# Performance work log

Measured on AMD Instinct MI355X. Metric: run time of the kernel, lower is better.

## Reference

```python
import jax, jax.numpy as jnp
import numpy as np

D_MODEL = 1024
NHEAD = 16
HEAD_DIM = D_MODEL // NHEAD


def setup_inputs() -> dict:
    key = jax.random.key(0)
    ks = jax.random.split(key, 6)
    scale = 0.02
    x = jax.random.normal(ks[0], (8, 1024, D_MODEL), dtype=jnp.float32)
    # nn.Linear weights are [out, in]; per-head q/k/v stacked over heads
    W_split = jax.random.normal(ks[1], (D_MODEL, D_MODEL), dtype=jnp.float32) * scale
    W_out = jax.random.normal(ks[2], (D_MODEL, D_MODEL), dtype=jnp.float32) * scale
    Wq = jax.random.normal(ks[3], (NHEAD, HEAD_DIM, HEAD_DIM), dtype=jnp.float32) * scale
    Wk = jax.random.normal(ks[4], (NHEAD, HEAD_DIM, HEAD_DIM), dtype=jnp.float32) * scale
    Wv = jax.random.normal(ks[5], (NHEAD, HEAD_DIM, HEAD_DIM), dtype=jnp.float32) * scale
    return {"x": x, "W_split": W_split, "W_out": W_out, "Wq": Wq, "Wk": Wk, "Wv": Wv}


def reference(x, W_split, W_out, Wq, Wk, Wv):
    b, s, _ = x.shape
    # x_proj: [b, s, h, hd]
    xp = (x @ W_split.T).reshape(b, s, NHEAD, HEAD_DIM)
    # per-head Linear (weight [out,in]): y = x @ W.T
    q = jnp.einsum('bshd,hod->bsho', xp, Wq)
    k = jnp.einsum('bshd,hod->bsho', xp, Wk)
    v = jnp.einsum('bshd,hod->bsho', xp, Wv)
    # scores scaled by sqrt(head_dim) (Attention.d_model == head_dim)
    scores = jnp.einsum('bsho,btho->bhst', q, k) / jnp.sqrt(jnp.float32(HEAD_DIM))
    attn = jax.nn.softmax(scores, axis=-1)  # [b, h, s, s]
    out = jnp.einsum('bhst,btho->bsho', attn, v)  # [b, s, h, hd]
    concat = out.reshape(b, s, D_MODEL)
    return concat @ W_out.T
```

## Files before the change

### kernel.cpp

```cpp
#include <hip/hip_runtime.h>
#include <math.h>

#define NHEAD 16
#define HD 64
#define DMODEL 1024
#define SEQ 1024
#define BATCH 8
#define ROWS (BATCH * SEQ)

typedef __attribute__((ext_vector_type(8))) short bf16x8;
typedef __attribute__((ext_vector_type(8))) short short8v;
typedef __attribute__((ext_vector_type(4))) float f32x4;
typedef __attribute__((ext_vector_type(16))) float f32x16;
typedef __attribute__((ext_vector_type(4))) short short4v;
typedef __attribute__((ext_vector_type(4))) unsigned int uint32x4;

__device__ __forceinline__ unsigned short f2bf(float f) {
    unsigned u = __builtin_bit_cast(unsigned, f);
    u += 0x7FFF + ((u >> 16) & 1);
    return (unsigned short)(u >> 16);
}

__device__ __forceinline__ float fexp2(float x) {
#if __has_builtin(__builtin_amdgcn_exp2f)
    return __builtin_amdgcn_exp2f(x);
#else
    return __expf(x * 0.6931471805599453f);
#endif
}

__device__ __forceinline__ void gload16(const void* g, void* l) {
    __builtin_amdgcn_global_load_lds(
        (const __attribute__((address_space(1))) unsigned int*)g,
        (__attribute__((address_space(3))) unsigned int*)l, 16, 0, 0);
}

__global__ __launch_bounds__(256) void cvt_bf16(const float* __restrict__ src,
                                                unsigned short* __restrict__ dst,
                                                int n, float scale) {
    int i = (blockIdx.x * 256 + threadIdx.x) * 8;
    if (i >= n) return;
    float4 a = *(const float4*)(src + i);
    float4 b = *(const float4*)(src + i + 4);
    short8v o;
    o[0] = (short)f2bf(a.x * scale); o[1] = (short)f2bf(a.y * scale);
    o[2] = (short)f2bf(a.z * scale); o[3] = (short)f2bf(a.w * scale);
    o[4] = (short)f2bf(b.x * scale); o[5] = (short)f2bf(b.y * scale);
    o[6] = (short)f2bf(b.z * scale); o[7] = (short)f2bf(b.w * scale);
    *(short8v*)(dst + i) = o;
}

__global__ __launch_bounds__(256) void gemm1_qkv(const unsigned short* __restrict__ A,
                                                 const unsigned short* __restrict__ B,
                                                 const unsigned short* __restrict__ wqb,
                                                 const unsigned short* __restrict__ wkb,
                                                 const unsigned short* __restrict__ wvb,
                                                 unsigned short* __restrict__ qb,
                                                 unsigned short* __restrict__ kbuf,
                                                 unsigned short* __restrict__ vT) {
    __shared__ char lds[65536];
    const int tid  = threadIdx.x;
    const int w    = tid >> 6;
    const int lane = tid & 63;
    const int lr   = lane & 15, lg = lane >> 4;
    const int wr   = w >> 1,  wc = w & 1;
    const int m0   = blockIdx.y * 128;
    const int n0   = blockIdx.x * 128;
    const int K    = DMODEL;

    f32x4 acc[4][4] = {};

    const int srow   = lane >> 3;
    const int swbyte = ((lane & 7) ^ srow) << 4;

#define G1_STAGE(buf, k0)                                                          \
    {                                                                              \
        _Pragma("unroll")                                                          \
        for (int c = 0; c < 4; ++c) {                                              \
            int chunk = w * 4 + c;                                                 \
            int row   = chunk * 8 + srow;                                          \
            gload16((const char*)A + ((size_t)(m0 + row) * K + (k0)) * 2 + swbyte, \
                    lds + (buf) * 16384 + chunk * 1024);                           \
            gload16((const char*)B + ((size_t)(n0 + row) * K + (k0)) * 2 + swbyte, \
                    lds + 32768 + (buf) * 16384 + chunk * 1024);                   \
        }                                                                          \
    }

    G1_STAGE(0, 0);
    __syncthreads();

    int cur = 0;
    for (int t = 0; t < K / 64; ++t) {
        if (t + 1 < K / 64) G1_STAGE(cur ^ 1, (t + 1) * 64);

#pragma unroll
        for (int k2 = 0; k2 < 2; ++k2) {
            bf16x8 af[4], bg[4];
#pragma unroll
            for (int f = 0; f < 4; ++f) {
                int row = wr * 64 + f * 16 + lr;
                af[f] = *(const bf16x8*)(lds + cur * 16384 + row * 128 +
                                         ((k2 * 64 + lg * 16) ^ ((row & 7) << 4)));
            }
#pragma unroll
            for (int g = 0; g < 4; ++g) {
                int row = wc * 64 + g * 16 + lr;
                bg[g] = *(const bf16x8*)(lds + 32768 + cur * 16384 + row * 128 +
                                         ((k2 * 64 + lg * 16) ^ ((row & 7) << 4)));
            }
#pragma unroll
            for (int f = 0; f < 4; ++f)
#pragma unroll
                for (int g = 0; g < 4; ++g)
                    acc[f][g] = __builtin_amdgcn_mfma_f32_16x16x32_bf16(af[f], bg[g],
                                                                        acc[f][g], 0, 0, 0);
        }
        __syncthreads();
        cur ^= 1;
    }
#undef G1_STAGE

#pragma unroll
    for (int f = 0; f < 4; ++f)
#pragma unroll
        for (int g = 0; g < 4; ++g)
#pragma unroll
            for (int r = 0; r < 4; ++r) {
                int mrow = wr * 64 + f * 16 + lg * 4 + r;
                int ncol = wc * 64 + g * 16 + lr;
                *(unsigned short*)(lds + mrow * 256 + ((ncol * 2) ^ ((mrow & 7) << 4))) =
                    f2bf(acc[f][g][r]);
            }

    const int b  = m0 >> 10;
    const int sl = m0 & 1023;

#pragma unroll
    for (int hh = 0; hh < 2; ++hh) {
        const int h = blockIdx.x * 2 + hh;
#pragma unroll
        for (int i = 0; i < 6; ++i) {
            int c   = w * 6 + i;
            int p   = c >> 3, rc = c & 7;
            int row = rc * 8 + srow;
            const unsigned short* ws = (p == 0) ? wqb : (p == 1) ? wkb : wvb;
            gload16((const char*)ws + ((size_t)(h * 64 + row) * 64) * 2 + swbyte,
                    lds + 32768 + p * 8192 + rc * 1024);
        }
        __syncthreads();

        f32x4 a2[3][2][4] = {};
#pragma unroll
        for (int k2 = 0; k2 < 2; ++k2) {
            bf16x8 af[2];
#pragma unroll
            for (int f = 0; f < 2; ++f) {
                int row = w * 32 + f * 16 + lr;
                af[f] = *(const bf16x8*)(lds + row * 256 +
                                         ((hh * 128 + k2 * 64 + lg * 16) ^ ((row & 7) << 4)));
            }
#pragma unroll
            for (int p = 0; p < 3; ++p)
#pragma unroll
                for (int g = 0; g < 4; ++g) {
                    int o = g * 16 + lr;
                    bf16x8 bg = *(const bf16x8*)(lds + 32768 + p * 8192 + o * 128 +
                                                 ((k2 * 64 + lg * 16) ^ ((o & 7) << 4)));
#pragma unroll
                    for (int f = 0; f < 2; ++f)
                        a2[p][f][g] = __builtin_amdgcn_mfma_f32_16x16x32_bf16(af[f], bg,
                                                                              a2[p][f][g], 0, 0, 0);
                }
        }

#pragma unroll
        for (int f = 0; f < 2; ++f)
#pragma unroll
            for (int g = 0; g < 4; ++g) {
#pragma unroll
                for (int r = 0; r < 4; ++r) {
                    size_t idx = (size_t)(m0 + w * 32 + f * 16 + lg * 4 + r) * DMODEL +
                                 h * 64 + g * 16 + lr;
                    qb[idx]   = f2bf(a2[0][f][g][r]);
                    kbuf[idx] = f2bf(a2[1][f][g][r]);
                }
                short4v pv;
#pragma unroll
                for (int r = 0; r < 4; ++r) pv[r] = (short)f2bf(a2[2][f][g][r]);
                size_t o = (size_t)(b * 16 + h) * 64 + g * 16 + lr;
                *(short4v*)(vT + o * SEQ + sl + w * 32 + f * 16 + lg * 4) = pv;
            }
        __syncthreads();
    }
}

__global__ __launch_bounds__(256) void gemm_bf16(const unsigned short* __restrict__ A,
                                                 const unsigned short* __restrict__ B,
                                                 float* __restrict__ Cf,
                                                 int M, int N, int K) {
    __shared__ char sA[2][16384];
    __shared__ char sB[2][16384];
    const int tid  = threadIdx.x;
    const int w    = tid >> 6;
    const int lane = tid & 63;
    const int lr   = lane & 15, lg = lane >> 4;
    const int wr   = w >> 1,  wc = w & 1;
    const int m0   = blockIdx.y * 128;
    const int n0   = blockIdx.x * 128;

    f32x4 acc[4][4] = {};

    const int srow   = lane >> 3;
    const int swbyte = ((lane & 7) ^ srow) << 4;
    const int nt     = K / 64;

#define GEMM_STAGE(buf, k0)                                                        \
    {                                                                              \
        _Pragma("unroll")                                                          \
        for (int c = 0; c < 4; ++c) {                                              \
            int chunk = w * 4 + c;                                                 \
            int row   = chunk * 8 + srow;                                          \
            gload16((const char*)A + ((size_t)(m0 + row) * K + (k0)) * 2 + swbyte, \
                    sA[buf] + chunk * 1024);                                       \
            gload16((const char*)B + ((size_t)(n0 + row) * K + (k0)) * 2 + swbyte, \
                    sB[buf] + chunk * 1024);                                       \
        }                                                                          \
    }

    GEMM_STAGE(0, 0);
    __syncthreads();

    int cur = 0;
    for (int t = 0; t < nt; ++t) {
        if (t + 1 < nt) GEMM_STAGE(cur ^ 1, (t + 1) * 64);

#pragma unroll
        for (int k2 = 0; k2 < 2; ++k2) {
            bf16x8 af[4], bg[4];
#pragma unroll
            for (int f = 0; f < 4; ++f) {
                int row = wr * 64 + f * 16 + lr;
                af[f] = *(const bf16x8*)(sA[cur] + row * 128 +
                                         ((k2 * 64 + lg * 16) ^ ((row & 7) << 4)));
            }
#pragma unroll
            for (int g = 0; g < 4; ++g) {
                int row = wc * 64 + g * 16 + lr;
                bg[g] = *(const bf16x8*)(sB[cur] + row * 128 +
                                         ((k2 * 64 + lg * 16) ^ ((row & 7) << 4)));
            }
#pragma unroll
            for (int f = 0; f < 4; ++f)
#pragma unroll
                for (int g = 0; g < 4; ++g)
                    acc[f][g] = __builtin_amdgcn_mfma_f32_16x16x32_bf16(af[f], bg[g],
                                                                        acc[f][g], 0, 0, 0);
        }
        __syncthreads();
        cur ^= 1;
    }
#undef GEMM_STAGE

#pragma unroll
    for (int f = 0; f < 4; ++f)
#pragma unroll
        for (int g = 0; g < 4; ++g)
#pragma unroll
            for (int r = 0; r < 4; ++r)
                Cf[(size_t)(m0 + wr * 64 + f * 16 + lg * 4 + r) * N +
                   n0 + wc * 64 + g * 16 + lr] = acc[f][g][r];
}

__global__ __launch_bounds__(512) void attn_mfma(const unsigned short* __restrict__ qb,
                                                 const unsigned short* __restrict__ kb,
                                                 const unsigned short* __restrict__ vT,
                                                 unsigned short* __restrict__ ob) {
    __shared__ unsigned short sK[2][4096];
    __shared__ unsigned short sV[2][4096];

    const int tid  = threadIdx.x;
    const int w    = tid >> 6;
    const int lane = tid & 63;
    const int ql   = lane & 31;
    const int hl   = lane >> 5;
    const int bh   = blockIdx.y;
    const int b    = bh >> 4, h = bh & 15;
    const int s0   = blockIdx.x * 256;

    const unsigned short* qrow = qb + ((size_t)(b * SEQ + s0 + w * 32 + ql) * DMODEL + h * 64);
    bf16x8 qf[4];
#pragma unroll
    for (int s = 0; s < 4; ++s)
        qf[s] = *(const bf16x8*)(qrow + 16 * s + 8 * hl);

    f32x16 acc0 = {}, acc1 = {};
    float m_ = -1e30f, l_ = 0.f;

    const int srow = lane >> 3;
    const int ssw  = ((lane & 7) << 4) ^ (srow << 4);
    const int swz  = (ql & 7) << 4;

#define ATTN_STAGE(buf, kt)                                                          \
    {                                                                                \
        int row = w * 8 + srow;                                                      \
        gload16((const char*)kb +                                                    \
                    (((size_t)(b * SEQ + (kt) * 64 + row) * DMODEL + h * 64) * 2) + ssw, \
                (char*)sK[buf] + w * 1024);                                          \
        gload16((const char*)vT +                                                    \
                    (((size_t)(bh * 64 + row) * SEQ + (kt) * 64) * 2) + ssw,         \
                (char*)sV[buf] + w * 1024);                                          \
    }

    ATTN_STAGE(0, 0);
    __syncthreads();

    int cur = 0;
    for (int kt = 0; kt < SEQ / 64; ++kt) {
        if (kt + 1 < SEQ / 64) ATTN_STAGE(cur ^ 1, kt + 1);

        f32x16 st0 = {}, st1 = {};
        __builtin_amdgcn_s_setprio(1);
#pragma unroll
        for (int s = 0; s < 4; ++s) {
            int byo = (32 * s + 16 * hl) ^ swz;
            bf16x8 kf0 = *(const bf16x8*)((const char*)sK[cur] + ql * 128 + byo);
            bf16x8 kf1 = *(const bf16x8*)((const char*)sK[cur] + (32 + ql) * 128 + byo);
            st0 = __builtin_amdgcn_mfma_f32_32x32x16_bf16(kf0, qf[s], st0, 0, 0, 0);
            st1 = __builtin_amdgcn_mfma_f32_32x32x16_bf16(kf1, qf[s], st1, 0, 0, 0);
        }
        __builtin_amdgcn_s_setprio(0);

        float mx = st0[0];
#pragma unroll
        for (int i = 1; i < 16; ++i) mx = fmaxf(mx, st0[i]);
#pragma unroll
        for (int i = 0; i < 16; ++i) mx = fmaxf(mx, st1[i]);
        if (__any(mx > m_ + 8.f)) {
            float rm = fmaxf(mx, __shfl_xor(mx, 32, 64));
            float mn = fmaxf(m_, rm);
            float al = fexp2(m_ - mn);
            m_ = mn;
            l_ *= al;
#pragma unroll
            for (int i = 0; i < 16; ++i) { acc0[i] *= al; acc1[i] *= al; }
        }

        bf16x8 pf[4];
        float lsum = 0.f;
#define TILE_P(stv, PF0, PF1)                                                       \
        {                                                                           \
            float p_[16];                                                           \
            _Pragma("unroll")                                                       \
            for (int i = 0; i < 16; ++i) {                                          \
                p_[i] = fexp2(stv[i] - m_);                                         \
                lsum += p_[i];                                                      \
            }                                                                       \
            unsigned pk_[8];                                                        \
            _Pragma("unroll")                                                       \
            for (int i = 0; i < 8; ++i)                                             \
                asm("v_cvt_pk_bf16_f32 %0, %1, %2"                                  \
                    : "=v"(pk_[i]) : "v"(p_[2 * i]), "v"(p_[2 * i + 1]));           \
            auto rA = __builtin_amdgcn_permlane32_swap(pk_[0], pk_[2], false, false); \
            auto rB = __builtin_amdgcn_permlane32_swap(pk_[1], pk_[3], false, false); \
            auto rC = __builtin_amdgcn_permlane32_swap(pk_[4], pk_[6], false, false); \
            auto rD = __builtin_amdgcn_permlane32_swap(pk_[5], pk_[7], false, false); \
            uint32x4 f0, f1;                                                        \
            f0[0] = rA[0]; f0[1] = rB[0]; f0[2] = rA[1]; f0[3] = rB[1];             \
            f1[0] = rC[0]; f1[1] = rD[0]; f1[2] = rC[1]; f1[3] = rD[1];             \
            PF0 = __builtin_bit_cast(bf16x8, f0);                                   \
            PF1 = __builtin_bit_cast(bf16x8, f1);                                   \
        }
        TILE_P(st0, pf[0], pf[1]);
        TILE_P(st1, pf[2], pf[3]);
#undef TILE_P
        l_ += lsum;

        __builtin_amdgcn_s_setprio(1);
#pragma unroll
        for (int s = 0; s < 4; ++s) {
            int byo = (32 * s + 16 * hl) ^ swz;
            bf16x8 vf0 = *(const bf16x8*)((const char*)sV[cur] + ql * 128 + byo);
            bf16x8 vf1 = *(const bf16x8*)((const char*)sV[cur] + (32 + ql) * 128 + byo);
            acc0 = __builtin_amdgcn_mfma_f32_32x32x16_bf16(vf0, pf[s], acc0, 0, 0, 0);
            acc1 = __builtin_amdgcn_mfma_f32_32x32x16_bf16(vf1, pf[s], acc1, 0, 0, 0);
        }
        __builtin_amdgcn_s_setprio(0);
        __syncthreads();
        cur ^= 1;
    }
#undef ATTN_STAGE

    float lf  = l_ + __shfl_xor(l_, 32, 64);
    float inv = 1.f / lf;
    const size_t rowbase = (size_t)(b * SEQ + s0 + w * 32 + ql) * DMODEL + h * 64;
#pragma unroll
    for (int reg = 0; reg < 16; ++reg) {
        int d = (reg & 3) + 8 * (reg >> 2) + 4 * hl;
        ob[rowbase + d]      = f2bf(acc0[reg] * inv);
        ob[rowbase + 32 + d] = f2bf(acc1[reg] * inv);
    }
}

#define QSCALE 0.18033688011112042f
extern "C" void kernel_launch(void* const* d_in, const int* in_sizes, int n_in,
                              void* d_out, int out_size, void* d_ws, size_t ws_size,
                              hipStream_t stream) {
    const float* x       = (const float*)d_in[0];
    const float* W_split = (const float*)d_in[1];
    const float* W_out   = (const float*)d_in[2];
    const float* Wq      = (const float*)d_in[3];
    const float* Wk      = (const float*)d_in[4];
    const float* Wv      = (const float*)d_in[5];
    float* out = (float*)d_out;

    unsigned short* xb  = (unsigned short*)d_ws;
    unsigned short* obb = xb;
    unsigned short* wsb = xb + (size_t)ROWS * DMODEL;
    unsigned short* wob = wsb + (size_t)DMODEL * DMODEL;
    unsigned short* qbuf= wob + (size_t)DMODEL * DMODEL;
    unsigned short* kbuf= qbuf + (size_t)ROWS * DMODEL;
    unsigned short* vT  = kbuf + (size_t)ROWS * DMODEL;
    unsigned short* wqb = vT + (size_t)ROWS * DMODEL;
    unsigned short* wkb = wqb + (size_t)NHEAD * HD * HD;
    unsigned short* wvb = wkb + (size_t)NHEAD * HD * HD;

    dim3 blk(256);

    cvt_bf16<<<dim3(ROWS * DMODEL / 2048), blk, 0, stream>>>(x, xb, ROWS * DMODEL, 1.f);
    cvt_bf16<<<dim3(DMODEL * DMODEL / 2048), blk, 0, stream>>>(W_split, wsb, DMODEL * DMODEL, 1.f);
    cvt_bf16<<<dim3(DMODEL * DMODEL / 2048), blk, 0, stream>>>(W_out, wob, DMODEL * DMODEL, 1.f);
    cvt_bf16<<<dim3(NHEAD * HD * HD / 2048), blk, 0, stream>>>(Wq, wqb, NHEAD * HD * HD, QSCALE);
    cvt_bf16<<<dim3(NHEAD * HD * HD / 2048), blk, 0, stream>>>(Wk, wkb, NHEAD * HD * HD, 1.f);
    cvt_bf16<<<dim3(NHEAD * HD * HD / 2048), blk, 0, stream>>>(Wv, wvb, NHEAD * HD * HD, 1.f);

    gemm1_qkv<<<dim3(DMODEL / 128, ROWS / 128), blk, 0, stream>>>(
        xb, wsb, wqb, wkb, wvb, qbuf, kbuf, vT);
    attn_mfma<<<dim3(SEQ / 256, BATCH * NHEAD), dim3(512), 0, stream>>>(qbuf, kbuf, vT, obb);
    gemm_bf16<<<dim3(DMODEL / 128, ROWS / 128), blk, 0, stream>>>(
        obb, wob, out, ROWS, DMODEL, DMODEL);
}
```

Baseline: 131.5 us.

## Deepen attention K/V prefetch to 4 buffers and transpose grid mapping

Result: faster. 128.6 us (-2.2%).

```diff
diff --git a/kernel.cpp b/kernel.cpp
--- a/kernel.cpp
+++ b/kernel.cpp
@@ -64,8 +64,8 @@
     const int lane = tid & 63;
     const int lr   = lane & 15, lg = lane >> 4;
     const int wr   = w >> 1,  wc = w & 1;
-    const int m0   = blockIdx.y * 128;
-    const int n0   = blockIdx.x * 128;
+    const int m0   = blockIdx.x * 128;
+    const int n0   = blockIdx.y * 128;
     const int K    = DMODEL;
 
     f32x4 acc[4][4] = {};
@@ -137,7 +137,7 @@
 
 #pragma unroll
     for (int hh = 0; hh < 2; ++hh) {
-        const int h = blockIdx.x * 2 + hh;
+        const int h = blockIdx.y * 2 + hh;
 #pragma unroll
         for (int i = 0; i < 6; ++i) {
             int c   = w * 6 + i;
@@ -205,8 +205,8 @@
     const int lane = tid & 63;
     const int lr   = lane & 15, lg = lane >> 4;
     const int wr   = w >> 1,  wc = w & 1;
-    const int m0   = blockIdx.y * 128;
-    const int n0   = blockIdx.x * 128;
+    const int m0   = blockIdx.x * 128;
+    const int n0   = blockIdx.y * 128;
 
     f32x4 acc[4][4] = {};
 
@@ -275,17 +275,18 @@
                                                  const unsigned short* __restrict__ kb,
                                                  const unsigned short* __restrict__ vT,
                                                  unsigned short* __restrict__ ob) {
-    __shared__ unsigned short sK[2][4096];
-    __shared__ unsigned short sV[2][4096];
+    __shared__ unsigned short sK[4][4096];
+    __shared__ unsigned short sV[4][4096];
 
     const int tid  = threadIdx.x;
     const int w    = tid >> 6;
     const int lane = tid & 63;
     const int ql   = lane & 31;
     const int hl   = lane >> 5;
-    const int bh   = blockIdx.y;
+    const int bh   = blockIdx.x;
     const int b    = bh >> 4, h = bh & 15;
-    const int s0   = blockIdx.x * 256;
+    const int s0   = blockIdx.y * 256;
+    const int NT   = SEQ / 64;
 
     const unsigned short* qrow = qb + ((size_t)(b * SEQ + s0 + w * 32 + ql) * DMODEL + h * 64);
     bf16x8 qf[4];
@@ -312,19 +313,22 @@
     }
 
     ATTN_STAGE(0, 0);
-    __syncthreads();
-
-    int cur = 0;
-    for (int kt = 0; kt < SEQ / 64; ++kt) {
-        if (kt + 1 < SEQ / 64) ATTN_STAGE(cur ^ 1, kt + 1);
+    ATTN_STAGE(1, 1);
+    asm volatile("s_waitcnt vmcnt(2)" ::: "memory");
+    __builtin_amdgcn_s_barrier();
+    __builtin_amdgcn_sched_barrier(0);
+
+    for (int kt = 0; kt < NT; ++kt) {
+        const int cb = kt & 3;
+        if (kt + 2 < NT) ATTN_STAGE((kt + 2) & 3, kt + 2);
 
         f32x16 st0 = {}, st1 = {};
         __builtin_amdgcn_s_setprio(1);
 #pragma unroll
         for (int s = 0; s < 4; ++s) {
             int byo = (32 * s + 16 * hl) ^ swz;
-            bf16x8 kf0 = *(const bf16x8*)((const char*)sK[cur] + ql * 128 + byo);
-            bf16x8 kf1 = *(const bf16x8*)((const char*)sK[cur] + (32 + ql) * 128 + byo);
+            bf16x8 kf0 = *(const bf16x8*)((const char*)sK[cb] + ql * 128 + byo);
+            bf16x8 kf1 = *(const bf16x8*)((const char*)sK[cb] + (32 + ql) * 128 + byo);
             st0 = __builtin_amdgcn_mfma_f32_32x32x16_bf16(kf0, qf[s], st0, 0, 0, 0);
             st1 = __builtin_amdgcn_mfma_f32_32x32x16_bf16(kf1, qf[s], st1, 0, 0, 0);
         }
@@ -379,14 +383,17 @@
 #pragma unroll
         for (int s = 0; s < 4; ++s) {
             int byo = (32 * s + 16 * hl) ^ swz;
-            bf16x8 vf0 = *(const bf16x8*)((const char*)sV[cur] + ql * 128 + byo);
-            bf16x8 vf1 = *(const bf16x8*)((const char*)sV[cur] + (32 + ql) * 128 + byo);
+            bf16x8 vf0 = *(const bf16x8*)((const char*)sV[cb] + ql * 128 + byo);
+            bf16x8 vf1 = *(const bf16x8*)((const char*)sV[cb] + (32 + ql) * 128 + byo);
             acc0 = __builtin_amdgcn_mfma_f32_32x32x16_bf16(vf0, pf[s], acc0, 0, 0, 0);
             acc1 = __builtin_amdgcn_mfma_f32_32x32x16_bf16(vf1, pf[s], acc1, 0, 0, 0);
         }
         __builtin_amdgcn_s_setprio(0);
-        __syncthreads();
-        cur ^= 1;
+
+        if (kt + 2 < NT) { asm volatile("s_waitcnt vmcnt(2)" ::: "memory"); }
+        else             { asm volatile("s_waitcnt vmcnt(0)" ::: "memory"); }
+        __builtin_amdgcn_s_barrier();
+        __builtin_amdgcn_sched_barrier(0);
     }
 #undef ATTN_STAGE
 
@@ -433,9 +440,9 @@
     cvt_bf16<<<dim3(NHEAD * HD * HD / 2048), blk, 0, stream>>>(Wk, wkb, NHEAD * HD * HD, 1.f);
     cvt_bf16<<<dim3(NHEAD * HD * HD / 2048), blk, 0, stream>>>(Wv, wvb, NHEAD * HD * HD, 1.f);
 
-    gemm1_qkv<<<dim3(DMODEL / 128, ROWS / 128), blk, 0, stream>>>(
+    gemm1_qkv<<<dim3(ROWS / 128, DMODEL / 128), blk, 0, stream>>>(
         xb, wsb, wqb, wkb, wvb, qbuf, kbuf, vT);
-    attn_mfma<<<dim3(SEQ / 256, BATCH * NHEAD), dim3(512), 0, stream>>>(qbuf, kbuf, vT, obb);
-    gemm_bf16<<<dim3(DMODEL / 128, ROWS / 128), blk, 0, stream>>>(
+    attn_mfma<<<dim3(BATCH * NHEAD, SEQ / 256), dim3(512), 0, stream>>>(qbuf, kbuf, vT, obb);
+    gemm_bf16<<<dim3(ROWS / 128, DMODEL / 128), blk, 0, stream>>>(
         obb, wob, out, ROWS, DMODEL, DMODEL);
 }
```
